# Kernel tuning notes

Hardware: AMD Instinct MI355X
Metric: run time of the kernel (lower is better)

The kernel has to match this reference:

```python
import jax, jax.numpy as jnp
import numpy as np

N_EXPERTS = 8
D_MODEL = 1024
D_FF = 4096
N_TOKENS = 2048
TOP_K = 2


def _init_expert_weight(key, shape):
    # torch init: bound = sqrt(3) * (sqrt(1/3) / sqrt(fan_in)) = 1/sqrt(fan_in), fan_in = shape[1]
    bound = 1.0 / np.sqrt(shape[1])
    return jax.random.uniform(key, shape, jnp.float32, -bound, bound)


def setup_inputs() -> dict:
    key = jax.random.key(0)
    kx, ki, kw, k1, k2, k3 = jax.random.split(key, 6)
    x = jax.random.normal(kx, (N_TOKENS, D_MODEL), jnp.float32)
    expert_indices = jax.random.randint(ki, (N_TOKENS, TOP_K), 0, N_EXPERTS, jnp.int32)
    expert_weights = jax.random.uniform(kw, (N_TOKENS, TOP_K), jnp.float32)
    w1 = _init_expert_weight(k1, (N_EXPERTS, D_MODEL, D_FF))
    w2 = _init_expert_weight(k2, (N_EXPERTS, D_MODEL, D_FF))
    w3 = _init_expert_weight(k3, (N_EXPERTS, D_FF, D_MODEL))
    return {"x": x, "expert_indices": expert_indices, "expert_weights": expert_weights,
            "w1": w1, "w2": w2, "w3": w3}


def reference(x, expert_indices, expert_weights, w1, w2, w3):
    n_tokens, d_model = x.shape
    top_k = expert_indices.shape[1]
    n_experts = w1.shape[0]
    A = n_tokens * top_k  # total assignments; static capacity per expert (no overflow possible)

    flat_e = expert_indices.reshape(-1)            # [A]
    flat_w = expert_weights.reshape(-1)            # [A]
    tok_idx = jnp.repeat(jnp.arange(n_tokens), top_k)  # [A]

    order = jnp.argsort(flat_e, stable=True)
    s_tok = tok_idx[order]
    s_e = flat_e[order]
    s_w = flat_w[order]

    counts = jnp.bincount(flat_e, length=n_experts)            # [E]
    seg_starts = jnp.concatenate([jnp.zeros((1,), counts.dtype), jnp.cumsum(counts)[:-1]])
    pos = jnp.arange(A) - seg_starts[s_e]                       # position within expert segment

    # dispatch: padded per-expert batch [E, A, d]
    padded = jnp.zeros((n_experts, A, d_model), x.dtype).at[s_e, pos].set(x[s_tok])

    gate = jax.nn.silu(jnp.einsum('ecd,edf->ecf', padded, w1))
    value = jnp.einsum('ecd,edf->ecf', padded, w2)
    hidden = gate * value
    expert_out = jnp.einsum('ecf,efd->ecd', hidden, w3)        # [E, A, d]

    # combine: gather per-assignment outputs, weight, scatter-add back to tokens
    y = expert_out[s_e, pos] * s_w[:, None]                    # [A, d]
    out = jnp.zeros((n_tokens, d_model), x.dtype).at[s_tok].add(y)
    return out
```

## Files before the change

kernel.cpp:

```cpp
#include <hip/hip_runtime.h>
#include <stdint.h>

#define N_EXPERTS 8
#define D_MODEL 1024
#define D_FF 4096
#define N_TOKENS 2048
#define ASSN 4096
#define ROWS 4224
#define BK 32

using bfrag = __attribute__((ext_vector_type(8))) short;
using f32x4 = __attribute__((ext_vector_type(4))) float;
typedef unsigned short u16;

__device__ __forceinline__ u16 f2bf(float f) {
  uint32_t u = __builtin_bit_cast(uint32_t, f);
  u += 0x7fffu + ((u >> 16) & 1u);
  return (u16)(u >> 16);
}

__device__ __forceinline__ void gll16(const void* g, void* l) {
  __builtin_amdgcn_global_load_lds(
      (const __attribute__((address_space(1))) void*)g,
      (__attribute__((address_space(3))) void*)l, 16, 0, 0);
}

__global__ void k_setup(const int* __restrict__ eidx, const float* __restrict__ ew,
                        int* __restrict__ rowmap, int* __restrict__ arow,
                        int* __restrict__ counts, int* __restrict__ offs) {
  __shared__ int sc[N_EXPERTS], so[N_EXPERTS];
  int t = threadIdx.x;
  if (t < N_EXPERTS) sc[t] = 0;
  __syncthreads();
  for (int a = t; a < ASSN; a += 256) atomicAdd(&sc[eidx[a]], 1);
  __syncthreads();
  if (t == 0) {
    int run = 0;
    for (int e = 0; e < N_EXPERTS; e++) {
      counts[e] = sc[e]; offs[e] = run; so[e] = run; run += sc[e];
    }
  }
  __syncthreads();
  for (int a = t; a < ASSN; a += 256) {
    int e = eidx[a];
    int p = atomicAdd(&so[e], 1);
    rowmap[p] = a;
    arow[a] = p;
  }
}

__global__ void k_gather(const float* __restrict__ x, const int* __restrict__ rowmap,
                         u16* __restrict__ Xg) {
  int r = blockIdx.x, t = threadIdx.x;
  uint2 o;
  if (r < ASSN) {
    int tok = rowmap[r] >> 1;
    float4 v = *(const float4*)(x + (size_t)tok * D_MODEL + t * 4);
    o.x = (uint32_t)f2bf(v.x) | ((uint32_t)f2bf(v.y) << 16);
    o.y = (uint32_t)f2bf(v.z) | ((uint32_t)f2bf(v.w) << 16);
  } else {
    o.x = 0u; o.y = 0u;
  }
  *(uint2*)(Xg + (size_t)r * D_MODEL + t * 4) = o;
}

__global__ void k_convt(const float* __restrict__ src, u16* __restrict__ dst,
                        int K, int N) {
  const int e = blockIdx.y;
  src += (size_t)e * K * N;
  dst += (size_t)e * K * N;
  const int ntn = N >> 6;
  const int n0 = (blockIdx.x % ntn) << 6;
  const int k0 = (blockIdx.x / ntn) << 6;
  __shared__ uint32_t T2[64 * 33];
  const int t = threadIdx.x;
  const int i4 = (t & 15) << 2;
  const int q  = t >> 4;
  #pragma unroll
  for (int p = 0; p < 2; p++) {
    const int kp = q + (p << 4);
    const float4 r0 = *(const float4*)(src + (size_t)(k0 + 2 * kp    ) * N + n0 + i4);
    const float4 r1 = *(const float4*)(src + (size_t)(k0 + 2 * kp + 1) * N + n0 + i4);
    T2[(i4 + 0) * 33 + kp] = (uint32_t)f2bf(r0.x) | ((uint32_t)f2bf(r1.x) << 16);
    T2[(i4 + 1) * 33 + kp] = (uint32_t)f2bf(r0.y) | ((uint32_t)f2bf(r1.y) << 16);
    T2[(i4 + 2) * 33 + kp] = (uint32_t)f2bf(r0.z) | ((uint32_t)f2bf(r1.z) << 16);
    T2[(i4 + 3) * 33 + kp] = (uint32_t)f2bf(r0.w) | ((uint32_t)f2bf(r1.w) << 16);
  }
  __syncthreads();
  const int n = t >> 2, seg = t & 3;
  uint32_t w[8];
  #pragma unroll
  for (int j = 0; j < 8; j++) w[j] = T2[n * 33 + (seg << 3) + j];
  u16* d = dst + (size_t)(n0 + n) * K + k0 + (seg << 4);
  *(uint4*)d = *(uint4*)&w[0];
  *(uint4*)(d + 8) = *(uint4*)&w[4];
}

__launch_bounds__(256, 2)
__global__ void k_gemm1(const u16* __restrict__ Xg,
                        const u16* __restrict__ w1t, const u16* __restrict__ w2t,
                        const int* __restrict__ counts, const int* __restrict__ offs,
                        u16* __restrict__ H) {
  const int e = blockIdx.z, nt = blockIdx.x, mt = blockIdx.y;
  const int cnt = counts[e];
  if (mt * 128 >= cnt) return;
  const int row0 = offs[e] + mt * 128;
  const int mrem = cnt - mt * 128;
  const int n0 = nt * 128;

  __shared__ u16 As[2][128 * BK];
  __shared__ u16 B1s[2][128 * BK];
  __shared__ u16 B2s[2][128 * BK];

  const int tid = threadIdx.x;
  const int lane = tid & 63, wave = tid >> 6;
  const int wm = (wave >> 1) << 6, wn = (wave & 1) << 6;
  const int l16 = lane & 15, quad = lane >> 4;

  const int srow = wave * 32 + (lane >> 2);
  const int scol = (lane & 3) * 8;
  const int ld0 = wave * 1024;

  const u16* pA  = Xg  + (size_t)(row0 + srow) * D_MODEL + scol;
  const u16* pB1 = w1t + (size_t)e * D_MODEL * D_FF + (size_t)(n0 + srow) * D_MODEL + scol;
  const u16* pB2 = w2t + (size_t)e * D_MODEL * D_FF + (size_t)(n0 + srow) * D_MODEL + scol;
  const size_t rstep = (size_t)16 * D_MODEL;

  f32x4 acc1[4][4] = {};
  f32x4 acc2[4][4] = {};

  gll16(pA,          &As[0][ld0]);
  gll16(pA + rstep,  &As[0][ld0 + 512]);
  gll16(pB1,         &B1s[0][ld0]);
  gll16(pB1 + rstep, &B1s[0][ld0 + 512]);
  gll16(pB2,         &B2s[0][ld0]);
  gll16(pB2 + rstep, &B2s[0][ld0 + 512]);
  pA += BK; pB1 += BK; pB2 += BK;

  #pragma unroll 2
  for (int ks = 0; ks < 32; ks++) {
    const int c = ks & 1;
    if (ks < 31) {
      gll16(pA,          &As[1 - c][ld0]);
      gll16(pA + rstep,  &As[1 - c][ld0 + 512]);
      gll16(pB1,         &B1s[1 - c][ld0]);
      gll16(pB1 + rstep, &B1s[1 - c][ld0 + 512]);
      gll16(pB2,         &B2s[1 - c][ld0]);
      gll16(pB2 + rstep, &B2s[1 - c][ld0 + 512]);
      pA += BK; pB1 += BK; pB2 += BK;
      asm volatile("s_waitcnt vmcnt(6)" ::: "memory");
    } else {
      asm volatile("s_waitcnt vmcnt(0)" ::: "memory");
    }
    __builtin_amdgcn_sched_barrier(0);
    __builtin_amdgcn_s_barrier();
    __builtin_amdgcn_sched_barrier(0);

    bfrag b1[4], b2[4];
    #pragma unroll
    for (int j = 0; j < 4; j++) {
      b1[j] = *(const bfrag*)&B1s[c][(wn + j * 16 + l16) * BK + quad * 8];
      b2[j] = *(const bfrag*)&B2s[c][(wn + j * 16 + l16) * BK + quad * 8];
    }
    #pragma unroll
    for (int i = 0; i < 4; i++) {
      bfrag a = *(const bfrag*)&As[c][(wm + i * 16 + l16) * BK + quad * 8];
      #pragma unroll
      for (int j = 0; j < 4; j++) {
        acc1[i][j] = __builtin_amdgcn_mfma_f32_16x16x32_bf16(a, b1[j], acc1[i][j], 0, 0, 0);
        acc2[i][j] = __builtin_amdgcn_mfma_f32_16x16x32_bf16(a, b2[j], acc2[i][j], 0, 0, 0);
      }
    }
    __builtin_amdgcn_sched_barrier(0);
    asm volatile("s_waitcnt lgkmcnt(0)" ::: "memory");
    __builtin_amdgcn_s_barrier();
    __builtin_amdgcn_sched_barrier(0);
  }

  #pragma unroll
  for (int i = 0; i < 4; i++) {
    #pragma unroll
    for (int p = 0; p < 4; p++) {
      const int mloc = wm + i * 16 + quad * 4 + p;
      if (mloc < mrem) {
        u16* dst = H + (size_t)(row0 + mloc) * D_FF + n0 + wn + l16;
        #pragma unroll
        for (int j = 0; j < 4; j++) {
          float g = acc1[i][j][p];
          float vv = acc2[i][j][p];
          float h = g / (1.0f + __expf(-g)) * vv;
          dst[j * 16] = f2bf(h);
        }
      }
    }
  }
}

__launch_bounds__(256, 2)
__global__ void k_gemm2(const u16* __restrict__ H, const u16* __restrict__ w3t,
                        const int* __restrict__ counts, const int* __restrict__ offs,
                        float* __restrict__ Y0, float* __restrict__ Y1) {
  const int e = blockIdx.z >> 1, khalf = blockIdx.z & 1;
  const int nt = blockIdx.x, mt = blockIdx.y;
  const int cnt = counts[e];
  if (mt * 128 >= cnt) return;
  const int row0 = offs[e] + mt * 128;
  const int mrem = cnt - mt * 128;
  const int n0 = nt * 128;
  float* __restrict__ Y = khalf ? Y1 : Y0;

  __shared__ u16 As[2][128 * BK];
  __shared__ u16 Bs[2][128 * BK];

  const int tid = threadIdx.x;
  const int lane = tid & 63, wave = tid >> 6;
  const int wm = (wave >> 1) << 6, wn = (wave & 1) << 6;
  const int l16 = lane & 15, quad = lane >> 4;

  const int srow = wave * 32 + (lane >> 2);
  const int scol = (lane & 3) * 8;
  const int ld0 = wave * 1024;

  const u16* pA = H + (size_t)(row0 + srow) * D_FF + khalf * 2048 + scol;
  const u16* pB = w3t + (size_t)e * D_FF * D_MODEL
                + (size_t)(n0 + srow) * D_FF + khalf * 2048 + scol;
  const size_t rstepA = (size_t)16 * D_FF;

  f32x4 acc[4][4] = {};

  gll16(pA,           &As[0][ld0]);
  gll16(pA + rstepA,  &As[0][ld0 + 512]);
  gll16(pB,           &Bs[0][ld0]);
  gll16(pB + rstepA,  &Bs[0][ld0 + 512]);
  pA += BK; pB += BK;

  #pragma unroll 2
  for (int ks = 0; ks < 64; ks++) {
    const int c = ks & 1;
    if (ks < 63) {
      gll16(pA,          &As[1 - c][ld0]);
      gll16(pA + rstepA, &As[1 - c][ld0 + 512]);
      gll16(pB,          &Bs[1 - c][ld0]);
      gll16(pB + rstepA, &Bs[1 - c][ld0 + 512]);
      pA += BK; pB += BK;
      asm volatile("s_waitcnt vmcnt(4)" ::: "memory");
    } else {
      asm volatile("s_waitcnt vmcnt(0)" ::: "memory");
    }
    __builtin_amdgcn_sched_barrier(0);
    __builtin_amdgcn_s_barrier();
    __builtin_amdgcn_sched_barrier(0);

    bfrag b[4];
    #pragma unroll
    for (int j = 0; j < 4; j++)
      b[j] = *(const bfrag*)&Bs[c][(wn + j * 16 + l16) * BK + quad * 8];
    #pragma unroll
    for (int i = 0; i < 4; i++) {
      bfrag a = *(const bfrag*)&As[c][(wm + i * 16 + l16) * BK + quad * 8];
      #pragma unroll
      for (int j = 0; j < 4; j++)
        acc[i][j] = __builtin_amdgcn_mfma_f32_16x16x32_bf16(a, b[j], acc[i][j], 0, 0, 0);
    }
    __builtin_amdgcn_sched_barrier(0);
    asm volatile("s_waitcnt lgkmcnt(0)" ::: "memory");
    __builtin_amdgcn_s_barrier();
    __builtin_amdgcn_sched_barrier(0);
  }

  #pragma unroll
  for (int i = 0; i < 4; i++) {
    #pragma unroll
    for (int p = 0; p < 4; p++) {
      const int mloc = wm + i * 16 + quad * 4 + p;
      if (mloc < mrem) {
        float* dst = Y + (size_t)(row0 + mloc) * D_MODEL + n0 + wn + l16;
        #pragma unroll
        for (int j = 0; j < 4; j++) dst[j * 16] = acc[i][j][p];
      }
    }
  }
}

__global__ void k_combine(const float* __restrict__ Y0, const float* __restrict__ Y1,
                          const int* __restrict__ arow, const float* __restrict__ ew,
                          float* __restrict__ out) {
  const int tk = blockIdx.x;
  const int d = threadIdx.x * 4;
  const int a0 = tk * 2, a1 = tk * 2 + 1;
  const int r0 = arow[a0], r1 = arow[a1];
  const float w0 = ew[a0], w1 = ew[a1];
  const float4 p0 = *(const float4*)(Y0 + (size_t)r0 * D_MODEL + d);
  const float4 q0 = *(const float4*)(Y1 + (size_t)r0 * D_MODEL + d);
  const float4 p1 = *(const float4*)(Y0 + (size_t)r1 * D_MODEL + d);
  const float4 q1 = *(const float4*)(Y1 + (size_t)r1 * D_MODEL + d);
  float4 r;
  r.x = w0 * (p0.x + q0.x) + w1 * (p1.x + q1.x);
  r.y = w0 * (p0.y + q0.y) + w1 * (p1.y + q1.y);
  r.z = w0 * (p0.z + q0.z) + w1 * (p1.z + q1.z);
  r.w = w0 * (p0.w + q0.w) + w1 * (p1.w + q1.w);
  *(float4*)(out + (size_t)tk * D_MODEL + d) = r;
}

extern "C" void kernel_launch(void* const* d_in, const int* in_sizes, int n_in,
                              void* d_out, int out_size, void* d_ws, size_t ws_size,
                              hipStream_t stream) {
  const float* x  = (const float*)d_in[0];
  const int* eidx = (const int*)d_in[1];
  const float* ew = (const float*)d_in[2];
  const float* w1 = (const float*)d_in[3];
  const float* w2 = (const float*)d_in[4];
  const float* w3 = (const float*)d_in[5];
  float* out = (float*)d_out;

  char* ws = (char*)d_ws;
  int*   rowmap = (int*)(ws);
  int*   arow   = (int*)(ws + 16384);
  int*   counts = (int*)(ws + 32768);
  int*   offs   = (int*)(ws + 32768 + 64);
  const size_t D0 = 65536;
  const size_t SZ_XG = (size_t)ROWS * D_MODEL * 2;
  const size_t SZ_HB = (size_t)ROWS * D_FF * 2;
  const size_t SZ_Y  = (size_t)ROWS * D_MODEL * 4;
  const size_t SZ_W  = (size_t)N_EXPERTS * D_MODEL * D_FF * 2;
  u16*   Xg  = (u16*)(ws + D0);
  u16*   Hb  = (u16*)(ws + D0 + SZ_XG);
  float* Y0  = (float*)(ws + D0 + SZ_XG + SZ_HB);
  float* Y1  = (float*)(ws + D0 + SZ_XG + SZ_HB + SZ_Y);
  u16*   wt1 = (u16*)(ws + D0 + SZ_XG + SZ_HB + 2 * SZ_Y);
  u16*   wt2 = wt1 + SZ_W / 2;
  u16*   wt3 = wt1;

  k_setup<<<1, 256, 0, stream>>>(eidx, ew, rowmap, arow, counts, offs);
  k_gather<<<ROWS, 256, 0, stream>>>(x, rowmap, Xg);
  k_convt<<<dim3(1024, N_EXPERTS), 256, 0, stream>>>(w1, wt1, D_MODEL, D_FF);
  k_convt<<<dim3(1024, N_EXPERTS), 256, 0, stream>>>(w2, wt2, D_MODEL, D_FF);
  k_gemm1<<<dim3(D_FF / 128, 32, N_EXPERTS), 256, 0, stream>>>(Xg, wt1, wt2, counts, offs, Hb);
  k_convt<<<dim3(1024, N_EXPERTS), 256, 0, stream>>>(w3, wt3, D_FF, D_MODEL);
  k_gemm2<<<dim3(D_MODEL / 128, 32, N_EXPERTS * 2), 256, 0, stream>>>(Hb, wt3, counts, offs, Y0, Y1);
  k_combine<<<N_TOKENS, 256, 0, stream>>>(Y0, Y1, arow, ew, out);
}
```

Before: 614.5 us.

## Enlarge GEMM tiles to 256x128 with BK=64, swizzled LDS and persistent convert blocks

Both expert GEMMs now use 512-thread blocks with 256-row M tiles and a K step of 64. The LDS layout is XOR-swizzled so fragment reads avoid bank conflicts, each K step is split into two halves with s_setprio raised around the MFMA bursts, and row padding grows to fit the larger tiles. The weight transpose-convert kernel now loops over eight K sub-tiles per block, so far fewer blocks are launched. The goal is more reuse per load and fewer LDS conflicts and barriers, at the cost of higher LDS and register pressure and more wasted rows in partial M tiles.

```diff
diff --git a/kernel.cpp b/kernel.cpp
--- a/kernel.cpp
+++ b/kernel.cpp
@@ -6,8 +6,8 @@
 #define D_FF 4096
 #define N_TOKENS 2048
 #define ASSN 4096
-#define ROWS 4224
-#define BK 32
+#define ROWS 4352
+#define BK 64
 
 using bfrag = __attribute__((ext_vector_type(8))) short;
 using f32x4 = __attribute__((ext_vector_type(4))) float;
@@ -66,89 +66,96 @@
 
 __global__ void k_convt(const float* __restrict__ src, u16* __restrict__ dst,
                         int K, int N) {
-  const int e = blockIdx.y;
+  const int e = blockIdx.z;
   src += (size_t)e * K * N;
   dst += (size_t)e * K * N;
-  const int ntn = N >> 6;
-  const int n0 = (blockIdx.x % ntn) << 6;
-  const int k0 = (blockIdx.x / ntn) << 6;
+  const int n0 = blockIdx.x << 6;
+  const int kbase = blockIdx.y << 9;
   __shared__ uint32_t T2[64 * 33];
   const int t = threadIdx.x;
   const int i4 = (t & 15) << 2;
   const int q  = t >> 4;
-  #pragma unroll
-  for (int p = 0; p < 2; p++) {
-    const int kp = q + (p << 4);
-    const float4 r0 = *(const float4*)(src + (size_t)(k0 + 2 * kp    ) * N + n0 + i4);
-    const float4 r1 = *(const float4*)(src + (size_t)(k0 + 2 * kp + 1) * N + n0 + i4);
-    T2[(i4 + 0) * 33 + kp] = (uint32_t)f2bf(r0.x) | ((uint32_t)f2bf(r1.x) << 16);
-    T2[(i4 + 1) * 33 + kp] = (uint32_t)f2bf(r0.y) | ((uint32_t)f2bf(r1.y) << 16);
-    T2[(i4 + 2) * 33 + kp] = (uint32_t)f2bf(r0.z) | ((uint32_t)f2bf(r1.z) << 16);
-    T2[(i4 + 3) * 33 + kp] = (uint32_t)f2bf(r0.w) | ((uint32_t)f2bf(r1.w) << 16);
-  }
-  __syncthreads();
   const int n = t >> 2, seg = t & 3;
-  uint32_t w[8];
-  #pragma unroll
-  for (int j = 0; j < 8; j++) w[j] = T2[n * 33 + (seg << 3) + j];
-  u16* d = dst + (size_t)(n0 + n) * K + k0 + (seg << 4);
-  *(uint4*)d = *(uint4*)&w[0];
-  *(uint4*)(d + 8) = *(uint4*)&w[4];
-}
-
-__launch_bounds__(256, 2)
+  for (int it = 0; it < 8; ++it) {
+    const int k0 = kbase + (it << 6);
+    if (it) __syncthreads();
+    #pragma unroll
+    for (int p = 0; p < 2; p++) {
+      const int kp = q + (p << 4);
+      const float4 r0 = *(const float4*)(src + (size_t)(k0 + 2 * kp    ) * N + n0 + i4);
+      const float4 r1 = *(const float4*)(src + (size_t)(k0 + 2 * kp + 1) * N + n0 + i4);
+      T2[(i4 + 0) * 33 + kp] = (uint32_t)f2bf(r0.x) | ((uint32_t)f2bf(r1.x) << 16);
+      T2[(i4 + 1) * 33 + kp] = (uint32_t)f2bf(r0.y) | ((uint32_t)f2bf(r1.y) << 16);
+      T2[(i4 + 2) * 33 + kp] = (uint32_t)f2bf(r0.z) | ((uint32_t)f2bf(r1.z) << 16);
+      T2[(i4 + 3) * 33 + kp] = (uint32_t)f2bf(r0.w) | ((uint32_t)f2bf(r1.w) << 16);
+    }
+    __syncthreads();
+    uint32_t w[8];
+    #pragma unroll
+    for (int j = 0; j < 8; j++) w[j] = T2[n * 33 + (seg << 3) + j];
+    u16* d = dst + (size_t)(n0 + n) * K + k0 + (seg << 4);
+    *(uint4*)d = *(uint4*)&w[0];
+    *(uint4*)(d + 8) = *(uint4*)&w[4];
+  }
+}
+
+__launch_bounds__(512, 2)
 __global__ void k_gemm1(const u16* __restrict__ Xg,
                         const u16* __restrict__ w1t, const u16* __restrict__ w2t,
                         const int* __restrict__ counts, const int* __restrict__ offs,
                         u16* __restrict__ H) {
   const int e = blockIdx.z, nt = blockIdx.x, mt = blockIdx.y;
   const int cnt = counts[e];
-  if (mt * 128 >= cnt) return;
-  const int row0 = offs[e] + mt * 128;
-  const int mrem = cnt - mt * 128;
+  if (mt * 256 >= cnt) return;
+  const int row0 = offs[e] + mt * 256;
+  const int mrem = cnt - mt * 256;
   const int n0 = nt * 128;
 
-  __shared__ u16 As[2][128 * BK];
+  __shared__ u16 As[2][256 * BK];
   __shared__ u16 B1s[2][128 * BK];
   __shared__ u16 B2s[2][128 * BK];
 
   const int tid = threadIdx.x;
   const int lane = tid & 63, wave = tid >> 6;
-  const int wm = (wave >> 1) << 6, wn = (wave & 1) << 6;
   const int l16 = lane & 15, quad = lane >> 4;
-
-  const int srow = wave * 32 + (lane >> 2);
-  const int scol = (lane & 3) * 8;
-  const int ld0 = wave * 1024;
-
-  const u16* pA  = Xg  + (size_t)(row0 + srow) * D_MODEL + scol;
-  const u16* pB1 = w1t + (size_t)e * D_MODEL * D_FF + (size_t)(n0 + srow) * D_MODEL + scol;
-  const u16* pB2 = w2t + (size_t)e * D_MODEL * D_FF + (size_t)(n0 + srow) * D_MODEL + scol;
-  const size_t rstep = (size_t)16 * D_MODEL;
+  const int wm = (wave >> 1) << 6;
+  const int wn = (wave & 1) << 6;
+
+  const int swz = ((lane & 7) ^ ((lane >> 3) & 7)) << 3;
+  const int arow = wave * 32 + (lane >> 3);
+  const int brow = wave * 16 + (lane >> 3);
+
+  const u16* pA  = Xg + (size_t)(row0 + arow) * D_MODEL + swz;
+  const size_t ebase = (size_t)e * D_MODEL * D_FF;
+  const u16* pB1 = w1t + ebase + (size_t)(n0 + brow) * D_MODEL + swz;
+  const u16* pB2 = w2t + ebase + (size_t)(n0 + brow) * D_MODEL + swz;
+
+  const int sA = l16 & 7;
+  const int slot0 = ((quad    ) ^ sA) << 3;
+  const int slot1 = ((quad + 4) ^ sA) << 3;
 
   f32x4 acc1[4][4] = {};
   f32x4 acc2[4][4] = {};
 
-  gll16(pA,          &As[0][ld0]);
-  gll16(pA + rstep,  &As[0][ld0 + 512]);
-  gll16(pB1,         &B1s[0][ld0]);
-  gll16(pB1 + rstep, &B1s[0][ld0 + 512]);
-  gll16(pB2,         &B2s[0][ld0]);
-  gll16(pB2 + rstep, &B2s[0][ld0 + 512]);
-  pA += BK; pB1 += BK; pB2 += BK;
-
-  #pragma unroll 2
-  for (int ks = 0; ks < 32; ks++) {
-    const int c = ks & 1;
-    if (ks < 31) {
-      gll16(pA,          &As[1 - c][ld0]);
-      gll16(pA + rstep,  &As[1 - c][ld0 + 512]);
-      gll16(pB1,         &B1s[1 - c][ld0]);
-      gll16(pB1 + rstep, &B1s[1 - c][ld0 + 512]);
-      gll16(pB2,         &B2s[1 - c][ld0]);
-      gll16(pB2 + rstep, &B2s[1 - c][ld0 + 512]);
-      pA += BK; pB1 += BK; pB2 += BK;
-      asm volatile("s_waitcnt vmcnt(6)" ::: "memory");
+#define STAGE1(buf)                                                  \
+  do {                                                               \
+    gll16(pA,                &As[buf][(wave * 32     ) * BK]);       \
+    gll16(pA +  8 * D_MODEL, &As[buf][(wave * 32 +  8) * BK]);       \
+    gll16(pA + 16 * D_MODEL, &As[buf][(wave * 32 + 16) * BK]);       \
+    gll16(pA + 24 * D_MODEL, &As[buf][(wave * 32 + 24) * BK]);       \
+    gll16(pB1,               &B1s[buf][(wave * 16    ) * BK]);       \
+    gll16(pB1 + 8 * D_MODEL, &B1s[buf][(wave * 16 + 8) * BK]);       \
+    gll16(pB2,               &B2s[buf][(wave * 16    ) * BK]);       \
+    gll16(pB2 + 8 * D_MODEL, &B2s[buf][(wave * 16 + 8) * BK]);       \
+    pA += BK; pB1 += BK; pB2 += BK;                                  \
+  } while (0)
+
+  STAGE1(0);
+  for (int t = 0; t < 16; ++t) {
+    const int c = t & 1;
+    if (t < 15) {
+      STAGE1(1 - c);
+      asm volatile("s_waitcnt vmcnt(8)" ::: "memory");
     } else {
       asm volatile("s_waitcnt vmcnt(0)" ::: "memory");
     }
@@ -156,26 +163,55 @@
     __builtin_amdgcn_s_barrier();
     __builtin_amdgcn_sched_barrier(0);
 
-    bfrag b1[4], b2[4];
+    bfrag a0[4], b10[4], b20[4];
+    #pragma unroll
+    for (int i = 0; i < 4; i++)
+      a0[i] = *(const bfrag*)&As[c][(wm + i * 16 + l16) * BK + slot0];
     #pragma unroll
     for (int j = 0; j < 4; j++) {
-      b1[j] = *(const bfrag*)&B1s[c][(wn + j * 16 + l16) * BK + quad * 8];
-      b2[j] = *(const bfrag*)&B2s[c][(wn + j * 16 + l16) * BK + quad * 8];
-    }
+      b10[j] = *(const bfrag*)&B1s[c][(wn + j * 16 + l16) * BK + slot0];
+      b20[j] = *(const bfrag*)&B2s[c][(wn + j * 16 + l16) * BK + slot0];
+    }
+    asm volatile("s_waitcnt lgkmcnt(0)" ::: "memory");
+    __builtin_amdgcn_sched_barrier(0);
+    __builtin_amdgcn_s_setprio(1);
     #pragma unroll
     for (int i = 0; i < 4; i++) {
-      bfrag a = *(const bfrag*)&As[c][(wm + i * 16 + l16) * BK + quad * 8];
       #pragma unroll
       for (int j = 0; j < 4; j++) {
-        acc1[i][j] = __builtin_amdgcn_mfma_f32_16x16x32_bf16(a, b1[j], acc1[i][j], 0, 0, 0);
-        acc2[i][j] = __builtin_amdgcn_mfma_f32_16x16x32_bf16(a, b2[j], acc2[i][j], 0, 0, 0);
+        acc1[i][j] = __builtin_amdgcn_mfma_f32_16x16x32_bf16(a0[i], b10[j], acc1[i][j], 0, 0, 0);
+        acc2[i][j] = __builtin_amdgcn_mfma_f32_16x16x32_bf16(a0[i], b20[j], acc2[i][j], 0, 0, 0);
       }
     }
-    __builtin_amdgcn_sched_barrier(0);
+    __builtin_amdgcn_s_setprio(0);
+
+    bfrag a1[4], b11[4], b21[4];
+    #pragma unroll
+    for (int i = 0; i < 4; i++)
+      a1[i] = *(const bfrag*)&As[c][(wm + i * 16 + l16) * BK + slot1];
+    #pragma unroll
+    for (int j = 0; j < 4; j++) {
+      b11[j] = *(const bfrag*)&B1s[c][(wn + j * 16 + l16) * BK + slot1];
+      b21[j] = *(const bfrag*)&B2s[c][(wn + j * 16 + l16) * BK + slot1];
+    }
     asm volatile("s_waitcnt lgkmcnt(0)" ::: "memory");
+    __builtin_amdgcn_sched_barrier(0);
+    __builtin_amdgcn_s_setprio(1);
+    #pragma unroll
+    for (int i = 0; i < 4; i++) {
+      #pragma unroll
+      for (int j = 0; j < 4; j++) {
+        acc1[i][j] = __builtin_amdgcn_mfma_f32_16x16x32_bf16(a1[i], b11[j], acc1[i][j], 0, 0, 0);
+        acc2[i][j] = __builtin_amdgcn_mfma_f32_16x16x32_bf16(a1[i], b21[j], acc2[i][j], 0, 0, 0);
+      }
+    }
+    __builtin_amdgcn_s_setprio(0);
+
+    __builtin_amdgcn_sched_barrier(0);
     __builtin_amdgcn_s_barrier();
     __builtin_amdgcn_sched_barrier(0);
   }
+#undef STAGE1
 
   #pragma unroll
   for (int i = 0; i < 4; i++) {
@@ -196,54 +232,59 @@
   }
 }
 
-__launch_bounds__(256, 2)
+__launch_bounds__(512, 2)
 __global__ void k_gemm2(const u16* __restrict__ H, const u16* __restrict__ w3t,
                         const int* __restrict__ counts, const int* __restrict__ offs,
                         float* __restrict__ Y0, float* __restrict__ Y1) {
   const int e = blockIdx.z >> 1, khalf = blockIdx.z & 1;
   const int nt = blockIdx.x, mt = blockIdx.y;
   const int cnt = counts[e];
-  if (mt * 128 >= cnt) return;
-  const int row0 = offs[e] + mt * 128;
-  const int mrem = cnt - mt * 128;
+  if (mt * 256 >= cnt) return;
+  const int row0 = offs[e] + mt * 256;
+  const int mrem = cnt - mt * 256;
   const int n0 = nt * 128;
   float* __restrict__ Y = khalf ? Y1 : Y0;
 
-  __shared__ u16 As[2][128 * BK];
+  __shared__ u16 As[2][256 * BK];
   __shared__ u16 Bs[2][128 * BK];
 
   const int tid = threadIdx.x;
   const int lane = tid & 63, wave = tid >> 6;
-  const int wm = (wave >> 1) << 6, wn = (wave & 1) << 6;
   const int l16 = lane & 15, quad = lane >> 4;
-
-  const int srow = wave * 32 + (lane >> 2);
-  const int scol = (lane & 3) * 8;
-  const int ld0 = wave * 1024;
-
-  const u16* pA = H + (size_t)(row0 + srow) * D_FF + khalf * 2048 + scol;
+  const int wm = (wave >> 1) << 6;
+  const int wn = (wave & 1) << 6;
+
+  const int swz = ((lane & 7) ^ ((lane >> 3) & 7)) << 3;
+  const int arow = wave * 32 + (lane >> 3);
+  const int brow = wave * 16 + (lane >> 3);
+
+  const u16* pA = H + (size_t)(row0 + arow) * D_FF + khalf * 2048 + swz;
   const u16* pB = w3t + (size_t)e * D_FF * D_MODEL
-                + (size_t)(n0 + srow) * D_FF + khalf * 2048 + scol;
-  const size_t rstepA = (size_t)16 * D_FF;
+                + (size_t)(n0 + brow) * D_FF + khalf * 2048 + swz;
+
+  const int sA = l16 & 7;
+  const int slot0 = ((quad    ) ^ sA) << 3;
+  const int slot1 = ((quad + 4) ^ sA) << 3;
 
   f32x4 acc[4][4] = {};
 
-  gll16(pA,           &As[0][ld0]);
-  gll16(pA + rstepA,  &As[0][ld0 + 512]);
-  gll16(pB,           &Bs[0][ld0]);
-  gll16(pB + rstepA,  &Bs[0][ld0 + 512]);
-  pA += BK; pB += BK;
-
-  #pragma unroll 2
-  for (int ks = 0; ks < 64; ks++) {
-    const int c = ks & 1;
-    if (ks < 63) {
-      gll16(pA,          &As[1 - c][ld0]);
-      gll16(pA + rstepA, &As[1 - c][ld0 + 512]);
-      gll16(pB,          &Bs[1 - c][ld0]);
-      gll16(pB + rstepA, &Bs[1 - c][ld0 + 512]);
-      pA += BK; pB += BK;
-      asm volatile("s_waitcnt vmcnt(4)" ::: "memory");
+#define STAGE2(buf)                                                  \
+  do {                                                               \
+    gll16(pA,               &As[buf][(wave * 32     ) * BK]);        \
+    gll16(pA +  8 * D_FF,   &As[buf][(wave * 32 +  8) * BK]);        \
+    gll16(pA + 16 * D_FF,   &As[buf][(wave * 32 + 16) * BK]);        \
+    gll16(pA + 24 * D_FF,   &As[buf][(wave * 32 + 24) * BK]);        \
+    gll16(pB,               &Bs[buf][(wave * 16    ) * BK]);         \
+    gll16(pB + 8 * D_FF,    &Bs[buf][(wave * 16 + 8) * BK]);         \
+    pA += BK; pB += BK;                                              \
+  } while (0)
+
+  STAGE2(0);
+  for (int t = 0; t < 32; ++t) {
+    const int c = t & 1;
+    if (t < 31) {
+      STAGE2(1 - c);
+      asm volatile("s_waitcnt vmcnt(6)" ::: "memory");
     } else {
       asm volatile("s_waitcnt vmcnt(0)" ::: "memory");
     }
@@ -251,22 +292,47 @@
     __builtin_amdgcn_s_barrier();
     __builtin_amdgcn_sched_barrier(0);
 
-    bfrag b[4];
+    bfrag a0[4], b0[4];
+    #pragma unroll
+    for (int i = 0; i < 4; i++)
+      a0[i] = *(const bfrag*)&As[c][(wm + i * 16 + l16) * BK + slot0];
     #pragma unroll
     for (int j = 0; j < 4; j++)
-      b[j] = *(const bfrag*)&Bs[c][(wn + j * 16 + l16) * BK + quad * 8];
+      b0[j] = *(const bfrag*)&Bs[c][(wn + j * 16 + l16) * BK + slot0];
+    asm volatile("s_waitcnt lgkmcnt(0)" ::: "memory");
+    __builtin_amdgcn_sched_barrier(0);
+    __builtin_amdgcn_s_setprio(1);
     #pragma unroll
     for (int i = 0; i < 4; i++) {
-      bfrag a = *(const bfrag*)&As[c][(wm + i * 16 + l16) * BK + quad * 8];
       #pragma unroll
       for (int j = 0; j < 4; j++)
-        acc[i][j] = __builtin_amdgcn_mfma_f32_16x16x32_bf16(a, b[j], acc[i][j], 0, 0, 0);
-    }
-    __builtin_amdgcn_sched_barrier(0);
+        acc[i][j] = __builtin_amdgcn_mfma_f32_16x16x32_bf16(a0[i], b0[j], acc[i][j], 0, 0, 0);
+    }
+    __builtin_amdgcn_s_setprio(0);
+
+    bfrag a1[4], b1[4];
+    #pragma unroll
+    for (int i = 0; i < 4; i++)
+      a1[i] = *(const bfrag*)&As[c][(wm + i * 16 + l16) * BK + slot1];
+    #pragma unroll
+    for (int j = 0; j < 4; j++)
+      b1[j] = *(const bfrag*)&Bs[c][(wn + j * 16 + l16) * BK + slot1];
     asm volatile("s_waitcnt lgkmcnt(0)" ::: "memory");
+    __builtin_amdgcn_sched_barrier(0);
+    __builtin_amdgcn_s_setprio(1);
+    #pragma unroll
+    for (int i = 0; i < 4; i++) {
+      #pragma unroll
+      for (int j = 0; j < 4; j++)
+        acc[i][j] = __builtin_amdgcn_mfma_f32_16x16x32_bf16(a1[i], b1[j], acc[i][j], 0, 0, 0);
+    }
+    __builtin_amdgcn_s_setprio(0);
+
+    __builtin_amdgcn_sched_barrier(0);
     __builtin_amdgcn_s_barrier();
     __builtin_amdgcn_sched_barrier(0);
   }
+#undef STAGE2
 
   #pragma unroll
   for (int i = 0; i < 4; i++) {
@@ -333,10 +399,10 @@
 
   k_setup<<<1, 256, 0, stream>>>(eidx, ew, rowmap, arow, counts, offs);
   k_gather<<<ROWS, 256, 0, stream>>>(x, rowmap, Xg);
-  k_convt<<<dim3(1024, N_EXPERTS), 256, 0, stream>>>(w1, wt1, D_MODEL, D_FF);
-  k_convt<<<dim3(1024, N_EXPERTS), 256, 0, stream>>>(w2, wt2, D_MODEL, D_FF);
-  k_gemm1<<<dim3(D_FF / 128, 32, N_EXPERTS), 256, 0, stream>>>(Xg, wt1, wt2, counts, offs, Hb);
-  k_convt<<<dim3(1024, N_EXPERTS), 256, 0, stream>>>(w3, wt3, D_FF, D_MODEL);
-  k_gemm2<<<dim3(D_MODEL / 128, 32, N_EXPERTS * 2), 256, 0, stream>>>(Hb, wt3, counts, offs, Y0, Y1);
+  k_convt<<<dim3(D_FF / 64, 2, N_EXPERTS), 256, 0, stream>>>(w1, wt1, D_MODEL, D_FF);
+  k_convt<<<dim3(D_FF / 64, 2, N_EXPERTS), 256, 0, stream>>>(w2, wt2, D_MODEL, D_FF);
+  k_gemm1<<<dim3(D_FF / 128, 16, N_EXPERTS), 512, 0, stream>>>(Xg, wt1, wt2, counts, offs, Hb);
+  k_convt<<<dim3(D_MODEL / 64, 8, N_EXPERTS), 256, 0, stream>>>(w3, wt3, D_FF, D_MODEL);
+  k_gemm2<<<dim3(D_MODEL / 128, 16, N_EXPERTS * 2), 512, 0, stream>>>(Hb, wt3, counts, offs, Y0, Y1);
   k_combine<<<N_TOKENS, 256, 0, stream>>>(Y0, Y1, arow, ew, out);
 }
```

After: 659.9 us. 7.4% more time.
